# Performance work log

Measured on AMD Instinct MI355X. Metric: run time of the kernel, lower is better.

## Reference

```python
import jax, jax.numpy as jnp
from jax import lax
import numpy as np

# ---- model dims ----
VOCAB, DMODEL, NLAYER = 32000, 1024, 4
NHEAD, HEAD = 16, 64              # RWKV6 heads (DMODEL = NHEAD*HEAD)
DIN = 2 * DMODEL                  # mamba expand=2
MHEAD, MHD = DIN // 64, 64        # mamba heads / head_dim (hard-coded 64 in block)
DSTATE, KCONV = 64, 4             # mamba2 state size / depthwise conv kernel
FFH = 4 * DMODEL
B, T = 1, 1024
EPS = 1e-6


def rmsnorm(v, w):
    return w * v * lax.rsqrt(jnp.mean(v * v, axis=-1, keepdims=True) + EPS)


def causal_dwconv(x, w):
    # x: [B,T,C], w: [C,K] depthwise causal conv
    C, K = w.shape
    xp = jnp.pad(x, ((0, 0), (K - 1, 0), (0, 0)))
    return lax.conv_general_dilated(
        xp, w.T[:, None, :], (1,), 'VALID',
        dimension_numbers=('NWC', 'WIO', 'NWC'), feature_group_count=C)


def setup_inputs() -> dict:
    key = jax.random.key(0)
    ks = iter(jax.random.split(key, 64))
    nrm = lambda shape, s=0.02: jax.random.normal(next(ks), shape, jnp.float32) * s
    x = jax.random.randint(next(ks), (B, T), 0, VOCAB)
    inp = dict(
        x=x,
        embed=nrm((VOCAB, DMODEL)),
        ln_w=jnp.ones((NLAYER, DMODEL), jnp.float32),
        Wr=nrm((NLAYER, DMODEL, DMODEL)), Wk=nrm((NLAYER, DMODEL, DMODEL)),
        Wv=nrm((NLAYER, DMODEL, DMODEL)), Ww=nrm((NLAYER, DMODEL, DMODEL)),
        w_bias=nrm((NLAYER, DMODEL), 0.5), u=nrm((NLAYER, NHEAD, HEAD), 0.5),
        Wg=nrm((NLAYER, DMODEL, DMODEL)), Wo=nrm((NLAYER, DMODEL, DMODEL)),
        Win=nrm((NLAYER, DMODEL, 2 * DIN + 2 * DSTATE + MHEAD)),
        conv_w=nrm((NLAYER, DIN + 2 * DSTATE, KCONV), 0.2),
        dt_bias=nrm((NLAYER, MHEAD), 0.5), A_log=nrm((NLAYER, MHEAD), 0.5),
        Dskip=nrm((NLAYER, MHEAD), 0.5),
        mnorm_w=jnp.ones((NLAYER, DIN), jnp.float32),
        Wout_m=nrm((NLAYER, DIN, DMODEL)),
        gate_w=nrm((NLAYER, 2 * DMODEL)), gate_b=jnp.zeros((NLAYER,), jnp.float32),
        ffn_ln_w=jnp.ones((NLAYER, DMODEL), jnp.float32),
        W1=nrm((NLAYER, DMODEL, FFH)), W2=nrm((NLAYER, FFH, DMODEL)),
        ln_out_w=jnp.ones((DMODEL,), jnp.float32),
    )
    return inp


def _block(h, p):
    (p_ln, pWr, pWk, pWv, pWw, p_wb, p_u, pWg, pWo, pWin, p_cw, p_dtb,
     p_Al, p_D, p_mn, pWom, p_gw, p_gb, p_fln, pW1, pW2) = p
    nx = rmsnorm(h, p_ln)

    # ---- RWKV6 linear attention ----
    r = (nx @ pWr).reshape(B, T, NHEAD, HEAD)
    k = (nx @ pWk).reshape(B, T, NHEAD, HEAD)
    v = (nx @ pWv).reshape(B, T, NHEAD, HEAD)
    dec = jnp.exp(-jnp.exp(nx @ pWw + p_wb)).reshape(B, T, NHEAD, HEAD)  # data-dep decay in (0,1)
    g = jax.nn.silu(nx @ pWg)

    def rstep(S, inp):
        rt, kt, vt, dt_ = inp                      # [B,H,hd]
        kv = kt[..., None] * vt[..., None, :]      # [B,H,hd,hd]
        o = jnp.einsum('bhk,bhkv->bhv', rt, S + p_u[None, :, :, None] * kv)
        return dt_[..., None] * S + kv, o

    S0 = jnp.zeros((B, NHEAD, HEAD, HEAD), nx.dtype)
    tmaj = lambda a: jnp.moveaxis(a, 1, 0)
    _, o = lax.scan(rstep, S0, (tmaj(r), tmaj(k), tmaj(v), tmaj(dec)))
    o = jnp.moveaxis(o, 0, 1).reshape(B, T, DMODEL)
    out_rwkv = (o * g) @ pWo

    # ---- Mamba2 selective scan ----
    zxbcdt = nx @ pWin
    z = zxbcdt[..., :DIN]
    xBC = zxbcdt[..., DIN:2 * DIN + 2 * DSTATE]
    dt = zxbcdt[..., -MHEAD:]
    xBC = jax.nn.silu(causal_dwconv(xBC, p_cw))
    xm = xBC[..., :DIN].reshape(B, T, MHEAD, MHD)
    Bm = xBC[..., DIN:DIN + DSTATE]
    Cm = xBC[..., DIN + DSTATE:]
    dt = jax.nn.softplus(dt + p_dtb)               # [B,T,MH]
    dA = jnp.exp(-dt * jnp.exp(p_Al))              # [B,T,MH]

    def mstep(hst, inp):
        xt, Bt, Ct, dAt, dtt = inp                 # [B,MH,hd],[B,ds],[B,ds],[B,MH],[B,MH]
        hst = dAt[..., None, None] * hst + (dtt[..., None] * xt)[..., None] * Bt[:, None, None, :]
        y = jnp.einsum('bhps,bs->bhp', hst, Ct)
        return hst, y

    h0 = jnp.zeros((B, MHEAD, MHD, DSTATE), nx.dtype)
    _, ym = lax.scan(mstep, h0, (tmaj(xm), tmaj(Bm), tmaj(Cm), tmaj(dA), tmaj(dt)))
    ym = jnp.moveaxis(ym, 0, 1) + p_D[None, None, :, None] * xm
    ym = ym.reshape(B, T, DIN)
    ym = rmsnorm(ym * jax.nn.silu(z), p_mn)        # gated RMSNorm
    out_mamba = ym @ pWom

    # ---- gated fusion + residual + FFN ----
    cat = jnp.concatenate([out_rwkv, out_mamba], axis=-1)
    gate = jax.nn.sigmoid(jnp.einsum('btd,d->bt', cat, p_gw) + p_gb)[..., None]
    h = h + gate * out_rwkv + (1.0 - gate) * out_mamba
    h = h + jax.nn.gelu(rmsnorm(h, p_fln) @ pW1, approximate=False) @ pW2
    return h


def reference(x, embed, ln_w, Wr, Wk, Wv, Ww, w_bias, u, Wg, Wo, Win, conv_w,
              dt_bias, A_log, Dskip, mnorm_w, Wout_m, gate_w, gate_b,
              ffn_ln_w, W1, W2, ln_out_w):
    h = embed[x]  # [B,T,D]
    params = (ln_w, Wr, Wk, Wv, Ww, w_bias, u, Wg, Wo, Win, conv_w, dt_bias,
              A_log, Dskip, mnorm_w, Wout_m, gate_w, gate_b, ffn_ln_w, W1, W2)
    h, _ = lax.scan(lambda c, p: (_block(c, p), None), h, params)
    logits = rmsnorm(h, ln_out_w) @ embed.T  # tied head
    return logits
```

## Files before the change

### kernel.cpp

```cpp
#include <hip/hip_runtime.h>
#include <hip/hip_bf16.h>
#include <math.h>

#define T 1024
#define NLAYER 4
#define NHEAD 16
#define HEAD 64
#define DIN 2048
#define MHEAD 32
#define DSTATE 64
#define FFH 4096
#define NWIN 4256
#define CCONV 2176
#define VOCABSZ 32000
#define NCHUNK 16
#define PKROWS 9472
#define PKN 9376

typedef unsigned short u16;
typedef __attribute__((ext_vector_type(8))) short s16x8;
typedef __attribute__((ext_vector_type(4))) float f32x4;

__device__ inline u16 f2bf(float f) {
  union { float f; unsigned u; } v; v.f = f;
// ... 73 lines not shown
  __shared__ float S[64][65];
  int w = blockIdx.z >> 2, l = blockIdx.z & 3;
  const float* sp = tc.src[w] + (size_t)l * 1024 * 1024;
  u16* dp = tc.dst[w] + (size_t)l * tc.dstride[w];
  int n0 = blockIdx.x * 64, k0 = blockIdx.y * 64;
  int tid = threadIdx.x;
  int tr = tid >> 4, tcc = (tid & 15) * 4;
  #pragma unroll
  for (int it = 0; it < 4; ++it) {
    int r = tr + it * 16;
    float4 v = *(const float4*)&sp[(size_t)(k0 + r) * 1024 + n0 + tcc];
    S[r][tcc + 0] = v.x; S[r][tcc + 1] = v.y; S[r][tcc + 2] = v.z; S[r][tcc + 3] = v.w;
  }
  __syncthreads();
  #pragma unroll
  for (int it = 0; it < 4; ++it) {
    int rn = tr + it * 16;
    u16 o[4];
    o[0] = f2bf(S[tcc + 0][rn]); o[1] = f2bf(S[tcc + 1][rn]);
    o[2] = f2bf(S[tcc + 2][rn]); o[3] = f2bf(S[tcc + 3][rn]);
    *(uint2*)&dp[(size_t)(n0 + rn) * 1024 + k0 + tcc] = *(uint2*)o;
  }
}

__global__ __launch_bounds__(256) void k_embln(const int* x, const float* embed,
                                               const float* w, float* h, u16* out) {
  __shared__ float sb[8];
  int t = blockIdx.x, tid = threadIdx.x;
  int row = x[t];
  float4 v = *(const float4*)&embed[(size_t)row * 1024 + tid * 4];
  *(float4*)&h[(size_t)t * 1024 + tid * 4] = v;
  float ss = v.x * v.x + v.y * v.y + v.z * v.z + v.w * v.w;
  float tot = block_sum(ss, sb);
  float rn = rsqrtf(tot / 1024.f + 1e-6f);
  int c = tid * 4;
  u16 o[4] = {f2bf(v.x * rn * w[c + 0]), f2bf(v.y * rn * w[c + 1]),
              f2bf(v.z * rn * w[c + 2]), f2bf(v.w * rn * w[c + 3])};
  *(uint2*)&out[(size_t)t * 1024 + c] = *(uint2*)o;
}

enum { EPI_F32 = 0, EPI_QKV = 1, EPI_GELU = 2 };

struct GOut {
  void* out;
  const float* aux;
  size_t zstride;
  float *r, *k, *v, *ld, *g, *zx;
};

template <int EPI, int BM, int BN>
__global__ __launch_bounds__(256) void k_gemm2(const u16* __restrict__ A,
                                               const u16* __restrict__ Bt,
                                               int N, int K, int kLen, GOut go) {
  __shared__ __align__(16) u16 As[2][BM][64];
  __shared__ __align__(16) u16 Bs[2][BN][64];
  constexpr int FR = BM / 32, FC = BN / 32;
  constexpr int LPS = BM / 32 + BN / 32;
  int tid = threadIdx.x, lane = tid & 63, wid = tid >> 6;
  int lid = blockIdx.y * gridDim.x + blockIdx.x;
  int nwg = gridDim.x * gridDim.y;
  int q = nwg >> 3, r8 = nwg & 7;
  int xcd = lid & 7, pos = lid >> 3;
  int wg = (xcd < r8) ? (xcd * (q + 1) + pos) : (r8 * (q + 1) + (xcd - r8) * q + pos);
  int m0 = (wg % gridDim.x) * BM, n0 = (wg / gridDim.x) * BN;
  int kOff = blockIdx.z * kLen;
  int wr = (wid >> 1) * (BM / 2), wc = (wid & 1) * (BN / 2);
  int lr = lane & 15, lk8 = (lane >> 4) * 8;
  int rsw = lr & 7;
  int swc = SWZ_SRC(lane);
  int rA = lane >> 3;
  f32x4 acc[FR][FC] = {};

  auto STAGE = [&](int buf, int k0) {
    #pragma unroll
    for (int it = 0; it < BM / 32; ++it) {
      int rb = wid * (BM / 4) + it * 8;
      gload16(&A[(size_t)(m0 + rb + rA) * K + k0 + swc], &As[buf][rb][0]);
    }
    #pragma unroll
    for (int it = 0; it < BN / 32; ++it) {
      int rb = wid * (BN / 4) + it * 8;
      gload16(&Bt[(size_t)(n0 + rb + rA) * K + k0 + swc], &Bs[buf][rb][0]);
    }
  };
  auto COMPUTE = [&](int buf) {
    #pragma unroll
    for (int kb = 0; kb < 64; kb += 32) {
      s16x8 af[FR], bf[FC];
      #pragma unroll
      for (int i = 0; i < FR; ++i)
        af[i] = *(const s16x8*)&As[buf][wr + i * 16 + lr][SWZ_RD(kb, lk8, rsw)];
      #pragma unroll
      for (int j = 0; j < FC; ++j)
        bf[j] = *(const s16x8*)&Bs[buf][wc + j * 16 + lr][SWZ_RD(kb, lk8, rsw)];
      #pragma unroll
      for (int i = 0; i < FR; ++i)
        #pragma unroll
        for (int j = 0; j < FC; ++j)
          acc[i][j] = __builtin_amdgcn_mfma_f32_16x16x32_bf16(af[i], bf[j], acc[i][j], 0, 0, 0);
    }
  };

  int nt = kLen >> 6;
  STAGE(0, kOff);
  int cur = 0;
  for (int t = 0; t < nt; ++t) {
    if (t + 1 < nt) {
      STAGE(cur ^ 1, kOff + (t + 1) * 64);
      asm volatile("s_waitcnt vmcnt(%0)" :: "n"(LPS) : "memory");
    } else {
      asm volatile("s_waitcnt vmcnt(0)" ::: "memory");
    }
    __builtin_amdgcn_s_barrier();
    __builtin_amdgcn_sched_barrier(0);
    COMPUTE(cur);
    __builtin_amdgcn_s_barrier();
    cur ^= 1;
  }

  float* outf = (float*)go.out + (size_t)blockIdx.z * go.zstride;
  #pragma unroll
  for (int i = 0; i < FR; ++i)
    #pragma unroll
    for (int j = 0; j < FC; ++j) {
      int row = m0 + wr + i * 16 + ((lane >> 4) << 2);
      int col = n0 + wc + j * 16 + lr;
      if (col >= N) continue;
      #pragma unroll
      for (int r_ = 0; r_ < 4; ++r_) {
        float v = acc[i][j][r_];
        size_t rr = (size_t)(row + r_);
        if constexpr (EPI == EPI_F32) {
          outf[rr * (size_t)N + col] = v;
        } else if constexpr (EPI == EPI_GELU) {
          ((u16*)go.out)[rr * (size_t)N + col] =
              f2bf(0.5f * v * (1.f + erff(v * 0.70710678118654752f)));
        } else if constexpr (EPI == EPI_QKV) {
          if (col < 1024)       go.r[rr * 1024 + col] = v;
          else if (col < 2048)  go.k[rr * 1024 + col - 1024] = v;
          else if (col < 3072)  go.v[rr * 1024 + col - 2048] = v;
          else if (col < 4096)  go.ld[rr * 1024 + col - 3072] = -expf(v + go.aux[col - 3072]);
          else if (col < 5120)  go.g[rr * 1024 + col - 4096] = v * sigf(v);
          else                  go.zx[rr * 4256 + col - 5120] = v;
        }
      }
    }
}

struct DualArg {
  const u16 *A0, *A1, *B0, *B1;
  float *o0, *o1;
  int K0, K1;
};
__global__ __launch_bounds__(256) void k_dual(DualArg da) {
  __shared__ __align__(16) u16 As[2][64][64];
  __shared__ __align__(16) u16 Bs[2][64][64];
  const u16* A  = blockIdx.z ? da.A1 : da.A0;
  const u16* Bt = blockIdx.z ? da.B1 : da.B0;
  float* out    = blockIdx.z ? da.o1 : da.o0;
  int K         = blockIdx.z ? da.K1 : da.K0;
  const int N = 1024;
  int tid = threadIdx.x, lane = tid & 63, wid = tid >> 6;
  int lid = blockIdx.y * gridDim.x + blockIdx.x;
  int nwg = gridDim.x * gridDim.y;
  int q = nwg >> 3, r8 = nwg & 7;
  int xcd = lid & 7, pos = lid >> 3;
  int wg = (xcd < r8) ? (xcd * (q + 1) + pos) : (r8 * (q + 1) + (xcd - r8) * q + pos);
  int m0 = (wg % gridDim.x) * 64, n0 = (wg / gridDim.x) * 64;
  int wr = (wid >> 1) * 32, wc = (wid & 1) * 32;
  int lr = lane & 15, lk8 = (lane >> 4) * 8;
  int rsw = lr & 7, swc = SWZ_SRC(lane), rA = lane >> 3;
  f32x4 acc[2][2] = {};
  auto STAGE = [&](int buf, int k0) {
    #pragma unroll
    for (int it = 0; it < 2; ++it) {
      int rb = wid * 16 + it * 8;
      gload16(&A[(size_t)(m0 + rb + rA) * K + k0 + swc], &As[buf][rb][0]);
      gload16(&Bt[(size_t)(n0 + rb + rA) * K + k0 + swc], &Bs[buf][rb][0]);
    }
  };
  auto COMPUTE = [&](int buf) {
    #pragma unroll
    for (int kb = 0; kb < 64; kb += 32) {
      s16x8 af[2], bf[2];
      #pragma unroll
      for (int i = 0; i < 2; ++i)
        af[i] = *(const s16x8*)&As[buf][wr + i * 16 + lr][SWZ_RD(kb, lk8, rsw)];
      #pragma unroll
      for (int j = 0; j < 2; ++j)
        bf[j] = *(const s16x8*)&Bs[buf][wc + j * 16 + lr][SWZ_RD(kb, lk8, rsw)];
      #pragma unroll
      for (int i = 0; i < 2; ++i)
        #pragma unroll
        for (int j = 0; j < 2; ++j)
          acc[i][j] = __builtin_amdgcn_mfma_f32_16x16x32_bf16(af[i], bf[j], acc[i][j], 0, 0, 0);
    }
  };
  int nt = K >> 6;
  STAGE(0, 0);
  int cur = 0;
  for (int t = 0; t < nt; ++t) {
    if (t + 1 < nt) {
      STAGE(cur ^ 1, (t + 1) * 64);
      asm volatile("s_waitcnt vmcnt(4)" ::: "memory");
    } else {
      asm volatile("s_waitcnt vmcnt(0)" ::: "memory");
    }
    __builtin_amdgcn_s_barrier();
    __builtin_amdgcn_sched_barrier(0);
    COMPUTE(cur);
    __builtin_amdgcn_s_barrier();
    cur ^= 1;
  }
  #pragma unroll
  for (int i = 0; i < 2; ++i)
    #pragma unroll
    for (int j = 0; j < 2; ++j) {
      int row = m0 + wr + i * 16 + ((lane >> 4) << 2);
      int col = n0 + wc + j * 16 + lr;
      #pragma unroll
      for (int r_ = 0; r_ < 4; ++r_)
        out[(size_t)(row + r_) * N + col] = acc[i][j][r_];
    }
}

__global__ void k_conv(const float* zx, const float* cw, float* xc) {
  int c = blockIdx.x * 256 + threadIdx.x;
  int t = blockIdx.y;
  if (c >= CCONV) return;
  float4 w = *(const float4*)&cw[c * 4];
  float acc = 0.f;
  if (t - 3 >= 0) acc += zx[(size_t)(t - 3) * NWIN + 2048 + c] * w.x;
  if (t - 2 >= 0) acc += zx[(size_t)(t - 2) * NWIN + 2048 + c] * w.y;
  if (t - 1 >= 0) acc += zx[(size_t)(t - 1) * NWIN + 2048 + c] * w.z;
  acc += zx[(size_t)t * NWIN + 2048 + c] * w.w;
  xc[(size_t)t * CCONV + c] = acc * sigf(acc);
}

__global__ __launch_bounds__(256) void k_dtbc(const float* __restrict__ zx,
                                              const float* __restrict__ xc,
                                              const float* __restrict__ dt_bias,
                                              const float* __restrict__ A_log,
                                              float* __restrict__ dtb, float* __restrict__ la,
                                              float* __restrict__ BC) {
  __shared__ float ldaS[64][33];
  __shared__ float Bc[64][65], Cc[64][65];
  int c = blockIdx.x, tid = threadIdx.x;
  #pragma unroll
  for (int it = 0; it < 8; ++it) {
    int e = it * 256 + tid;
    int i = e >> 5, j = e & 31;
    float x = zx[(size_t)(c * 64 + i) * NWIN + 4224 + j] + dt_bias[j];
    float sp = (x > 20.f) ? x : log1pf(expf(x));
    dtb[(size_t)(c * 64 + i) * 32 + j] = sp;
    ldaS[i][j] = -sp * expf(A_log[j]);
  }
  #pragma unroll
  for (int it = 0; it < 4; ++it) {
    int idx = it * 256 + tid;
    int r = idx >> 4, c4 = (idx & 15) * 4;
    float4 b4 = *(const float4*)&xc[(size_t)(c * 64 + r) * CCONV + 2048 + c4];
    float4 cv = *(const float4*)&xc[(size_t)(c * 64 + r) * CCONV + 2112 + c4];
    Bc[r][c4] = b4.x; Bc[r][c4+1] = b4.y; Bc[r][c4+2] = b4.z; Bc[r][c4+3] = b4.w;
    Cc[r][c4] = cv.x; Cc[r][c4+1] = cv.y; Cc[r][c4+2] = cv.z; Cc[r][c4+3] = cv.w;
  }
  __syncthreads();
  if (tid < 32) {
    float g = 0.f;
    for (int i = 0; i < 64; ++i) {
      g += ldaS[i][tid];
      la[((size_t)c * 32 + tid) * 64 + i] = g;
    }
  }
  int i = tid & 63, sg = tid >> 6;
  float acc[16] = {};
  for (int d = 0; d < 64; ++d) {
    float cv = Cc[i][d];
    #pragma unroll
    for (int j = 0; j < 16; ++j) acc[j] += Bc[sg * 16 + j][d] * cv;
  }
  #pragma unroll
  for (int j = 0; j < 16; ++j)
    BC[((size_t)c * 64 + i) * 64 + sg * 16 + j] = acc[j];
}

union SmemH1 {
  struct { float rS[64][66], kS[64][66], gS[64][66]; u16 khS[64][64]; u16 vtS[64][72]; float uS[64]; } a;
  struct { u16 XT[64][72], BT[64][72]; float fS[64]; } b;
};
__global__ __launch_bounds__(256) void k_heads1(const float* __restrict__ rbuf,
                                                const float* __restrict__ kbuf,
                                                const float* __restrict__ ldbuf,
                                                const float* __restrict__ vbuf,
                                                const float* __restrict__ u,
                                                const float* __restrict__ xc,
                                                const float* __restrict__ la,
                                                const float* __restrict__ dtb,
                                                u16* __restrict__ rt, float* __restrict__ eL,
                                                u16* __restrict__ G, float* __restrict__ U,
                                                float* __restrict__ Um) {
  __shared__ SmemH1 sm;
  int c = blockIdx.x, tid = threadIdx.x;
  int lane = tid & 63, wid = tid >> 6;
  int lr = lane & 15, lk8 = (lane >> 4) * 8, rsw = lr & 7;
  int wr = (wid >> 1) * 32, wc = (wid & 1) * 32;
  if (blockIdx.y < 16) {
    int h = blockIdx.y;
    #pragma unroll
    for (int it = 0; it < 4; ++it) {
      int idx = it * 256 + tid;
      int i = idx >> 4, c4 = (idx & 15) * 4;
      size_t base = (size_t)(c * 64 + i) * 1024 + h * 64 + c4;
      float4 rv = *(const float4*)&rbuf[base];
      float4 kv = *(const float4*)&kbuf[base];
      float4 lv = *(const float4*)&ldbuf[base];
      float4 vv = *(const float4*)&vbuf[base];
      sm.a.rS[i][c4] = rv.x; sm.a.rS[i][c4+1] = rv.y; sm.a.rS[i][c4+2] = rv.z; sm.a.rS[i][c4+3] = rv.w;
      sm.a.kS[i][c4] = kv.x; sm.a.kS[i][c4+1] = kv.y; sm.a.kS[i][c4+2] = kv.z; sm.a.kS[i][c4+3] = kv.w;
      sm.a.gS[i][c4] = lv.x; sm.a.gS[i][c4+1] = lv.y; sm.a.gS[i][c4+2] = lv.z; sm.a.gS[i][c4+3] = lv.w;
      sm.a.vtS[c4 + 0][i] = f2bf(vv.x); sm.a.vtS[c4 + 1][i] = f2bf(vv.y);
      sm.a.vtS[c4 + 2][i] = f2bf(vv.z); sm.a.vtS[c4 + 3][i] = f2bf(vv.w);
    }
    if (tid < 64) sm.a.uS[tid] = u[h * 64 + tid];
    __syncthreads();
    if (tid < 64) {
      int k = tid;
      float g = 0.f;
      for (int i = 0; i < 64; ++i) {
        float ld = sm.a.gS[i][k];
        sm.a.gS[i][k] = g;
        rt[(size_t)(c * 64 + i) * 1024 + h * 64 + k] = f2bf(sm.a.rS[i][k] * expf(g));
        g += ld;
      }
      float gL = g;
      eL[((size_t)c * 16 + h) * 64 + k] = expf(gL);
      for (int i = 0; i < 64; ++i) {
        float gincl = (i < 63) ? sm.a.gS[i + 1][k] : gL;
        int col = (((i >> 3) ^ (k & 7)) << 3) | (i & 7);
        sm.a.khS[k][col] = f2bf(sm.a.kS[i][k] * expf(fminf(gL - gincl, 0.f)));
      }
    }
    __syncthreads();
    {
      int i = tid & 63, sg = tid >> 6;
      float acc[16] = {};
      float accd = 0.f;
      for (int k = 0; k < 64; ++k) {
        float rv = sm.a.rS[i][k], gi = sm.a.gS[i][k];
        accd += rv * sm.a.uS[k] * sm.a.kS[i][k];
        #pragma unroll
        for (int j = 0; j < 16; ++j) {
          int s = sg * 16 + j;
          int sp1 = (s < 63) ? s + 1 : 63;
          acc[j] += rv * sm.a.kS[s][k] * expf(fminf(gi - sm.a.gS[sp1][k], 0.f));
        }
      }
      #pragma unroll
      for (int j = 0; j < 16; ++j) {
        int s = sg * 16 + j;
        float v = (s < i) ? acc[j] : ((s == i) ? accd : 0.f);
        G[(((size_t)c * 16 + h) * 64 + i) * 64 + s] = f2bf(v);
      }
    }
    {
      size_t gb = ((size_t)c * 16 + h) * 64;
      f32x4 acc2[2][2] = {};
      #pragma unroll
      for (int kb = 0; kb < 64; kb += 32) {
        s16x8 a[2], b[2];
        #pragma unroll
        for (int i_ = 0; i_ < 2; ++i_)
          a[i_] = *(const s16x8*)&sm.a.khS[wr + i_ * 16 + lr][SWZ_RD(kb, lk8, rsw)];
        #pragma unroll
        for (int j_ = 0; j_ < 2; ++j_)
          b[j_] = *(const s16x8*)&sm.a.vtS[wc + j_ * 16 + lr][kb + lk8];
        #pragma unroll
        for (int i_ = 0; i_ < 2; ++i_)
          #pragma unroll
          for (int j_ = 0; j_ < 2; ++j_)
            acc2[i_][j_] = __builtin_amdgcn_mfma_f32_16x16x32_bf16(a[i_], b[j_], acc2[i_][j_], 0, 0, 0);
      }
      #pragma unroll
      for (int i_ = 0; i_ < 2; ++i_)
        #pragma unroll
        for (int j_ = 0; j_ < 2; ++j_) {
          int row = wr + i_ * 16 + ((lane >> 4) << 2);
          int col = wc + j_ * 16 + lr;
          #pragma unroll
          for (int r_ = 0; r_ < 4; ++r_)
            U[(gb + row + r_) * 64 + col] = acc2[i_][j_][r_];
        }
    }
  } else {
    int h = blockIdx.y - 16;
    size_t lb = ((size_t)c * 32 + h) * 64;
    if (tid < 64) {
      float la63 = la[lb + 63];
      sm.b.fS[tid] = dtb[(size_t)(c * 64 + tid) * 32 + h] * expf(fminf(la63 - la[lb + tid], 0.f));
    }
    __syncthreads();
    #pragma unroll
    for (int it = 0; it < 4; ++it) {
      int idx = it * 256 + tid;
      int t = idx >> 4, p4 = (idx & 15) * 4;
      float f = sm.b.fS[t];
      float4 xv = *(const float4*)&xc[(size_t)(c * 64 + t) * CCONV + h * 64 + p4];
      sm.b.XT[p4 + 0][t] = f2bf(f * xv.x); sm.b.XT[p4 + 1][t] = f2bf(f * xv.y);
      sm.b.XT[p4 + 2][t] = f2bf(f * xv.z); sm.b.XT[p4 + 3][t] = f2bf(f * xv.w);
      float4 bv = *(const float4*)&xc[(size_t)(c * 64 + t) * CCONV + 2048 + p4];
      sm.b.BT[p4 + 0][t] = f2bf(bv.x); sm.b.BT[p4 + 1][t] = f2bf(bv.y);
      sm.b.BT[p4 + 2][t] = f2bf(bv.z); sm.b.BT[p4 + 3][t] = f2bf(bv.w);
    }
    __syncthreads();
    f32x4 acc[2][2] = {};
    #pragma unroll
    for (int kb = 0; kb < 64; kb += 32) {
      s16x8 a[2], b[2];
      #pragma unroll
      for (int i = 0; i < 2; ++i) a[i] = *(const s16x8*)&sm.b.XT[wr + i * 16 + lr][kb + lk8];
      #pragma unroll
      for (int j = 0; j < 2; ++j) b[j] = *(const s16x8*)&sm.b.BT[wc + j * 16 + lr][kb + lk8];
      #pragma unroll
      for (int i = 0; i < 2; ++i)
        #pragma unroll
        for (int j = 0; j < 2; ++j)
          acc[i][j] = __builtin_amdgcn_mfma_f32_16x16x32_bf16(a[i], b[j], acc[i][j], 0, 0, 0);
    }
    #pragma unroll
    for (int i = 0; i < 2; ++i)
      #pragma unroll
      for (int j = 0; j < 2; ++j) {
        int row = wr + i * 16 + ((lane >> 4) << 2);
        int col = wc + j * 16 + lr;
        #pragma unroll
        for (int r_ = 0; r_ < 4; ++r_)
          Um[(lb + row + r_) * 64 + col] = acc[i][j][r_];
      }
  }
}

__global__ __launch_bounds__(256) void k_scan2(const float* __restrict__ Urw,
                                               const float* __restrict__ eL,
                                               u16* __restrict__ Sall,
                                               const float* __restrict__ Um,
                                               const float* __restrict__ la,
                                               u16* __restrict__ hall) {
  int tid = threadIdx.x;
  if (blockIdx.x < 16) {
    int h = blockIdx.x;
    int k = tid >> 2, v0 = blockIdx.y * 16 + (tid & 3) * 4;
    float S[4] = {};
    for (int c = 0; c < 16; ++c) {
      size_t gb = ((size_t)c * 16 + h) * 64;
      u16 tmp[4] = {f2bf(S[0]), f2bf(S[1]), f2bf(S[2]), f2bf(S[3])};
      *(uint2*)&Sall[(gb + k) * 64 + v0] = *(uint2*)&tmp[0];
      float e = eL[gb + k];
      float4 uv = *(const float4*)&Urw[(gb + k) * 64 + v0];
      S[0] = e * S[0] + uv.x; S[1] = e * S[1] + uv.y;
      S[2] = e * S[2] + uv.z; S[3] = e * S[3] + uv.w;
    }
  } else {
    int h = blockIdx.x - 16;
    int p = tid >> 2, s0 = blockIdx.y * 16 + (tid & 3) * 4;
    float S[4] = {};
    for (int c = 0; c < 16; ++c) {
      size_t lb = ((size_t)c * 32 + h) * 64;
      u16 tmp[4] = {f2bf(S[0]), f2bf(S[1]), f2bf(S[2]), f2bf(S[3])};
      *(uint2*)&hall[(lb + p) * 64 + s0] = *(uint2*)&tmp[0];
      float e = expf(la[lb + 63]);
      float4 uv = *(const float4*)&Um[(lb + p) * 64 + s0];
      S[0] = e * S[0] + uv.x; S[1] = e * S[1] + uv.y;
      S[2] = e * S[2] + uv.z; S[3] = e * S[3] + uv.w;
    }
  }
}

union SmemH2 {
  struct { u16 rtS[64][64], GS[64][64], StS[64][72], vtS[64][72]; } a;
  struct { u16 MS[64][64], hS[64][64], CtS[64][72], XT2[64][72]; float laS[64], dtbS[64], eS[64]; } b;
};
__global__ __launch_bounds__(256) void k_heads2(const u16* __restrict__ rt,
                                                const u16* __restrict__ Gb,
                                                const u16* __restrict__ Sall,
                                                const float* __restrict__ vbuf,
                                                const float* __restrict__ gbuf,
                                                u16* __restrict__ og,
                                                const u16* __restrict__ hall,
                                                const float* __restrict__ xc,
                                                const float* __restrict__ la,
                                                const float* __restrict__ dtb,
                                                const float* __restrict__ BC,
                                                float* __restrict__ ymb) {
  __shared__ SmemH2 sm;
  int c = blockIdx.x, tid = threadIdx.x;
  int lane = tid & 63, wid = tid >> 6;
  int lr = lane & 15, lk8 = (lane >> 4) * 8;
  int rsw = lr & 7, swc = SWZ_SRC(lane);
  int wr = (wid >> 1) * 32, wc = (wid & 1) * 32;
  if (blockIdx.y < 16) {
    int h = blockIdx.y;
    size_t gb = ((size_t)c * 16 + h) * 64;
    #pragma unroll
    for (int it = 0; it < 2; ++it) {
      int rb = wid * 16 + it * 8;
      int r = rb + (lane >> 3);
      gload16(&rt[(size_t)(c * 64 + r) * 1024 + h * 64 + swc], &sm.a.rtS[rb][0]);
      gload16(&Gb[(gb + r) * 64 + swc], &sm.a.GS[rb][0]);
    }
    #pragma unroll
    for (int it = 0; it < 2; ++it) {
      int idx = it * 256 + tid;
      int k = idx >> 3, c8 = (idx & 7) * 8;
      uint4 ld = *(const uint4*)&Sall[(gb + k) * 64 + c8];
      const u16* pv = (const u16*)&ld;
      #pragma unroll
      for (int jj = 0; jj < 8; ++jj) sm.a.StS[c8 + jj][k] = pv[jj];
    }
    #pragma unroll
    for (int it = 0; it < 4; ++it) {
      int idx = it * 256 + tid;
      int s = idx >> 4, v4 = (idx & 15) * 4;
      float4 vv = *(const float4*)&vbuf[(size_t)(c * 64 + s) * 1024 + h * 64 + v4];
      sm.a.vtS[v4 + 0][s] = f2bf(vv.x); sm.a.vtS[v4 + 1][s] = f2bf(vv.y);
      sm.a.vtS[v4 + 2][s] = f2bf(vv.z); sm.a.vtS[v4 + 3][s] = f2bf(vv.w);
    }
    __syncthreads();
    f32x4 acc[2][2] = {};
    #pragma unroll
    for (int kb = 0; kb < 64; kb += 32) {
      s16x8 aR[2], aG[2], bS[2], bV[2];
      #pragma unroll
      for (int i = 0; i < 2; ++i) {
        aR[i] = *(const s16x8*)&sm.a.rtS[wr + i * 16 + lr][SWZ_RD(kb, lk8, rsw)];
        aG[i] = *(const s16x8*)&sm.a.GS[wr + i * 16 + lr][SWZ_RD(kb, lk8, rsw)];
      }
      #pragma unroll
      for (int j = 0; j < 2; ++j) {
        bS[j] = *(const s16x8*)&sm.a.StS[wc + j * 16 + lr][kb + lk8];
        bV[j] = *(const s16x8*)&sm.a.vtS[wc + j * 16 + lr][kb + lk8];
      }
      #pragma unroll
      for (int i = 0; i < 2; ++i)
        #pragma unroll
        for (int j = 0; j < 2; ++j) {
          acc[i][j] = __builtin_amdgcn_mfma_f32_16x16x32_bf16(aR[i], bS[j], acc[i][j], 0, 0, 0);
          acc[i][j] = __builtin_amdgcn_mfma_f32_16x16x32_bf16(aG[i], bV[j], acc[i][j], 0, 0, 0);
        }
    }
    #pragma unroll
    for (int i = 0; i < 2; ++i)
      #pragma unroll
      for (int j = 0; j < 2; ++j) {
        int row = c * 64 + wr + i * 16 + ((lane >> 4) << 2);
        int col = h * 64 + wc + j * 16 + lr;
        #pragma unroll
        for (int r_ = 0; r_ < 4; ++r_) {
          size_t idx = (size_t)(row + r_) * 1024 + col;
          og[idx] = f2bf(acc[i][j][r_] * gbuf[idx]);
        }
      }
  } else {
    int h = blockIdx.y - 16;
    size_t lb = ((size_t)c * 32 + h) * 64;
    if (tid < 64) {
      float lv = la[lb + tid];
      sm.b.laS[tid] = lv;
      sm.b.eS[tid] = expf(lv);
      sm.b.dtbS[tid] = dtb[(size_t)(c * 64 + tid) * 32 + h];
    }
    #pragma unroll
    for (int it = 0; it < 2; ++it) {
      int rb = wid * 16 + it * 8;
      int r = rb + (lane >> 3);
      gload16(&hall[(lb + r) * 64 + swc], &sm.b.hS[rb][0]);
    }
    __syncthreads();
    #pragma unroll
    for (int it = 0; it < 4; ++it) {
      int idx = it * 256 + tid;
      int i = idx >> 4, s4 = (idx & 15) * 4;
      float lai = sm.b.laS[i];
      float4 bc4 = *(const float4*)&BC[((size_t)c * 64 + i) * 64 + s4];
      u16 mo[4];
      #pragma unroll
      for (int j = 0; j < 4; ++j) {
        int s = s4 + j;
        float bcv = (j == 0) ? bc4.x : (j == 1) ? bc4.y : (j == 2) ? bc4.z : bc4.w;
        float v = 0.f;
        if (s <= i)
          v = expf(fminf(lai - sm.b.laS[s], 0.f)) * sm.b.dtbS[s] * bcv;
        mo[j] = f2bf(v);
      }
      *(uint2*)&sm.b.MS[i][(((s4 >> 3) ^ (i & 7)) << 3) | (s4 & 7)] = *(uint2*)mo;
      float ei = sm.b.eS[i];
      float4 cv = *(const float4*)&xc[(size_t)(c * 64 + i) * CCONV + 2112 + s4];
      sm.b.CtS[i][s4 + 0] = f2bf(ei * cv.x); sm.b.CtS[i][s4 + 1] = f2bf(ei * cv.y);
      sm.b.CtS[i][s4 + 2] = f2bf(ei * cv.z); sm.b.CtS[i][s4 + 3] = f2bf(ei * cv.w);
      float4 xv = *(const float4*)&xc[(size_t)(c * 64 + i) * CCONV + h * 64 + s4];
      sm.b.XT2[s4 + 0][i] = f2bf(xv.x); sm.b.XT2[s4 + 1][i] = f2bf(xv.y);
      sm.b.XT2[s4 + 2][i] = f2bf(xv.z); sm.b.XT2[s4 + 3][i] = f2bf(xv.w);
    }
    __syncthreads();
    f32x4 acc[2][2] = {};
    #pragma unroll
    for (int kb = 0; kb < 64; kb += 32) {
      s16x8 aM[2], aC[2], bX[2], bH[2];
      #pragma unroll
      for (int i = 0; i < 2; ++i) {
        aM[i] = *(const s16x8*)&sm.b.MS[wr + i * 16 + lr][SWZ_RD(kb, lk8, rsw)];
        aC[i] = *(const s16x8*)&sm.b.CtS[wr + i * 16 + lr][kb + lk8];
      }
      #pragma unroll
      for (int j = 0; j < 2; ++j) {
        bX[j] = *(const s16x8*)&sm.b.XT2[wc + j * 16 + lr][kb + lk8];
        bH[j] = *(const s16x8*)&sm.b.hS[wc + j * 16 + lr][SWZ_RD(kb, lk8, rsw)];
      }
      #pragma unroll
      for (int i = 0; i < 2; ++i)
        #pragma unroll
        for (int j = 0; j < 2; ++j) {
          acc[i][j] = __builtin_amdgcn_mfma_f32_16x16x32_bf16(aM[i], bX[j], acc[i][j], 0, 0, 0);
          acc[i][j] = __builtin_amdgcn_mfma_f32_16x16x32_bf16(aC[i], bH[j], acc[i][j], 0, 0, 0);
        }
    }
    #pragma unroll
    for (int i = 0; i < 2; ++i)
      #pragma unroll
      for (int j = 0; j < 2; ++j) {
        int row = c * 64 + wr + i * 16 + ((lane >> 4) << 2);
        int col = h * 64 + wc + j * 16 + lr;
        #pragma unroll
        for (int r_ = 0; r_ < 4; ++r_)
          ymb[(size_t)(row + r_) * 2048 + col] = acc[i][j][r_];
      }
  }
}

__global__ __launch_bounds__(256) void k_ymn(const float* ymb, const float* xc,
                                             const float* zx, const float* Dsk,
                                             const float* mnw, u16* out) {
  __shared__ float sb[8];
  int t = blockIdx.x, tid = threadIdx.x;
  float vals[8];
// ... 118 lines not shown
  float* rbuf     = (float*)alloc((size_t)T * 1024 * 4);
  float* kbuf     = (float*)alloc((size_t)T * 1024 * 4);
  float* vbuf     = (float*)alloc((size_t)T * 1024 * 4);
  float* ldbuf    = (float*)alloc((size_t)T * 1024 * 4);
  float* gbuf     = (float*)alloc((size_t)T * 1024 * 4);
  float* zx       = (float*)alloc((size_t)T * NWIN * 4);
  u16*   rt       = (u16*)alloc((size_t)T * 1024 * 2);
  float* eL       = (float*)alloc((size_t)NCHUNK * 16 * 64 * 4);
  u16*   Gb       = (u16*)alloc((size_t)NCHUNK * 16 * 64 * 64 * 2);
  float* Urw      = (float*)alloc((size_t)NCHUNK * 16 * 64 * 64 * 4);
  u16*   Sall     = (u16*)alloc((size_t)NCHUNK * 16 * 64 * 64 * 2);
  u16*   og       = (u16*)alloc((size_t)T * 1024 * 2);
  float* out_rwkv = (float*)alloc((size_t)T * 1024 * 4);
  float* xc       = (float*)alloc((size_t)T * CCONV * 4);
  float* dtb      = (float*)alloc((size_t)T * 32 * 4);
  float* la       = (float*)alloc((size_t)NCHUNK * 32 * 64 * 4);
  float* BC       = (float*)alloc((size_t)NCHUNK * 64 * 64 * 4);
  float* Um       = (float*)alloc((size_t)NCHUNK * 32 * 64 * 64 * 4);
  u16*   hall     = (u16*)alloc((size_t)NCHUNK * 32 * 64 * 64 * 2);
  float* ymb      = (float*)alloc((size_t)T * 2048 * 4);
  u16*   ymn      = (u16*)alloc((size_t)T * 2048 * 2);
  float* out_mam  = (float*)alloc((size_t)T * 1024 * 4);
  u16*   ffa      = (u16*)alloc((size_t)T * FFH * 2);
  float* part     = (float*)alloc((size_t)4 * 1024 * 1024 * 4);

  const size_t PKS = (size_t)PKROWS * 1024;

  k_cast<<<VOCABSZ * 1024 / 1024, 256, 0, stream>>>(embed, embB);
  {
    TC6 tc;
    tc.src[0] = Wr; tc.src[1] = Wk; tc.src[2] = Wv; tc.src[3] = Ww; tc.src[4] = Wg; tc.src[5] = Wo;
    tc.dst[0] = Wpk;               tc.dstride[0] = PKS;
    tc.dst[1] = Wpk + 1024 * 1024; tc.dstride[1] = PKS;
    tc.dst[2] = Wpk + 2048 * 1024; tc.dstride[2] = PKS;
    tc.dst[3] = Wpk + 3072 * 1024; tc.dstride[3] = PKS;
    tc.dst[4] = Wpk + 4096 * 1024; tc.dstride[4] = PKS;
    tc.dst[5] = WoT;               tc.dstride[5] = (size_t)1024 * 1024;
    k_tcast6<<<dim3(16, 16, 24), 256, 0, stream>>>(tc);
  }
  k_tcast<<<dim3(67, 16, 4), 256, 0, stream>>>(Win, (size_t)1024 * NWIN, Wpk + (size_t)5120 * 1024, PKS, 1024, NWIN);
  k_tcast<<<dim3(16, 32, 4), 256, 0, stream>>>(Wout_m, (size_t)2048 * 1024, WomT, (size_t)1024 * 2048, 2048, 1024);
  k_tcast<<<dim3(64, 16, 4), 256, 0, stream>>>(W1, (size_t)1024 * 4096, W1T, (size_t)4096 * 1024, 1024, 4096);
  k_tcast<<<dim3(16, 64, 4), 256, 0, stream>>>(W2, (size_t)4096 * 1024, W2T, (size_t)1024 * 4096, 4096, 1024);

  k_embln<<<1024, 256, 0, stream>>>(x, embed, ln_w, h, nx);

  for (int l = 0; l < NLAYER; ++l) {
    {
      GOut go = {};
      go.r = rbuf; go.k = kbuf; go.v = vbuf; go.ld = ldbuf; go.g = gbuf; go.zx = zx;
      go.aux = w_bias + l * 1024;
      k_gemm2<EPI_QKV, 128, 128><<<dim3(8, 74), 256, 0, stream>>>(nx, Wpk + (size_t)l * PKS, PKN, 1024, 1024, go);
    }
    k_conv<<<dim3(9, 1024), 256, 0, stream>>>(zx, conv_w + (size_t)l * CCONV * 4, xc);
    k_dtbc<<<16, 256, 0, stream>>>(zx, xc, dt_bias + l * 32, A_log + l * 32, dtb, la, BC);
    k_heads1<<<dim3(16, 48), 256, 0, stream>>>(rbuf, kbuf, ldbuf, vbuf, u + (size_t)l * 1024,
                                               xc, la, dtb, rt, eL, Gb, Urw, Um);
    k_scan2<<<dim3(48, 4), 256, 0, stream>>>(Urw, eL, Sall, Um, la, hall);
    k_heads2<<<dim3(16, 48), 256, 0, stream>>>(rt, Gb, Sall, vbuf, gbuf, og,
                                               hall, xc, la, dtb, BC, ymb);
    k_ymn<<<1024, 256, 0, stream>>>(ymb, xc, zx, Dskip + l * 32, mnorm_w + (size_t)l * 2048, ymn);
    {
      DualArg da;
      da.A0 = og;  da.B0 = WoT + (size_t)l * 1024 * 1024;  da.o0 = out_rwkv; da.K0 = 1024;
      da.A1 = ymn; da.B1 = WomT + (size_t)l * 1024 * 2048; da.o1 = out_mam;  da.K1 = 2048;
      k_dual<<<dim3(16, 16, 2), 256, 0, stream>>>(da);
    }
    k_gateln<<<1024, 256, 0, stream>>>(out_rwkv, out_mam, gate_w + (size_t)l * 2048,
                                       gate_b + l, h, ffn_ln + l * 1024, nx);
    {
      GOut go = {}; go.out = ffa;
      k_gemm2<EPI_GELU, 128, 128><<<dim3(8, 32), 256, 0, stream>>>(nx, W1T + (size_t)l * 4096 * 1024, 4096, 1024, 1024, go);
    }
    {
      GOut go = {}; go.out = part; go.zstride = (size_t)1024 * 1024;
      k_gemm2<EPI_F32, 64, 64><<<dim3(16, 16, 4), 256, 0, stream>>>(ffa, W2T + (size_t)l * 1024 * 4096, 1024, 4096, 1024, go);
    }
    k_redln<<<1024, 256, 0, stream>>>(part, h,
                                      (l < NLAYER - 1) ? (ln_w + (l + 1) * 1024) : ln_out, nx);
  }

  {
    GOut go = {}; go.out = d_out;
    k_gemm2<EPI_F32, 128, 128><<<dim3(8, 250), 256, 0, stream>>>(nx, embB, VOCABSZ, 1024, 1024, go);
  }
}
```

Before: 1.215 ms.

## Stage GEMM epilogues through shared memory, vectorize conv, split dtbc, use fast exp

GEMM kernels now merge their A and B shared buffers into one array. That array is reused after the main loop to stage the accumulator tile, so the epilogue can write coalesced float4 or bf16x4 rows instead of scattered scalar stores. The depthwise conv handles four channels per thread with float4 loads and stores. The dtbc kernel is split into five blocks per chunk so the B·C product is spread across more workgroups. Several expf calls in the scan kernels become __expf, which may cost some accuracy.

```diff
diff --git a/kernel.cpp b/kernel.cpp
--- a/kernel.cpp
+++ b/kernel.cpp
@@ -149,8 +149,7 @@
 __global__ __launch_bounds__(256) void k_gemm2(const u16* __restrict__ A,
                                                const u16* __restrict__ Bt,
                                                int N, int K, int kLen, GOut go) {
-  __shared__ __align__(16) u16 As[2][BM][64];
-  __shared__ __align__(16) u16 Bs[2][BN][64];
+  __shared__ __align__(16) u16 smem[2][BM + BN][64];
   constexpr int FR = BM / 32, FC = BN / 32;
   constexpr int LPS = BM / 32 + BN / 32;
   int tid = threadIdx.x, lane = tid & 63, wid = tid >> 6;
@@ -172,12 +171,12 @@
     #pragma unroll
     for (int it = 0; it < BM / 32; ++it) {
       int rb = wid * (BM / 4) + it * 8;
-      gload16(&A[(size_t)(m0 + rb + rA) * K + k0 + swc], &As[buf][rb][0]);
+      gload16(&A[(size_t)(m0 + rb + rA) * K + k0 + swc], &smem[buf][rb][0]);
     }
     #pragma unroll
     for (int it = 0; it < BN / 32; ++it) {
       int rb = wid * (BN / 4) + it * 8;
-      gload16(&Bt[(size_t)(n0 + rb + rA) * K + k0 + swc], &Bs[buf][rb][0]);
+      gload16(&Bt[(size_t)(n0 + rb + rA) * K + k0 + swc], &smem[buf][BM + rb][0]);
     }
   };
   auto COMPUTE = [&](int buf) {
@@ -186,10 +185,10 @@
       s16x8 af[FR], bf[FC];
       #pragma unroll
       for (int i = 0; i < FR; ++i)
-        af[i] = *(const s16x8*)&As[buf][wr + i * 16 + lr][SWZ_RD(kb, lk8, rsw)];
+        af[i] = *(const s16x8*)&smem[buf][wr + i * 16 + lr][SWZ_RD(kb, lk8, rsw)];
       #pragma unroll
       for (int j = 0; j < FC; ++j)
-        bf[j] = *(const s16x8*)&Bs[buf][wc + j * 16 + lr][SWZ_RD(kb, lk8, rsw)];
+        bf[j] = *(const s16x8*)&smem[buf][BM + wc + j * 16 + lr][SWZ_RD(kb, lk8, rsw)];
       #pragma unroll
       for (int i = 0; i < FR; ++i)
         #pragma unroll
@@ -215,33 +214,86 @@
     cur ^= 1;
   }
 
-  float* outf = (float*)go.out + (size_t)blockIdx.z * go.zstride;
+  __syncthreads();
+  float* cbuf = (float*)&smem[0][0][0];
   #pragma unroll
   for (int i = 0; i < FR; ++i)
     #pragma unroll
     for (int j = 0; j < FC; ++j) {
-      int row = m0 + wr + i * 16 + ((lane >> 4) << 2);
-      int col = n0 + wc + j * 16 + lr;
-      if (col >= N) continue;
-      #pragma unroll
-      for (int r_ = 0; r_ < 4; ++r_) {
-        float v = acc[i][j][r_];
-        size_t rr = (size_t)(row + r_);
-        if constexpr (EPI == EPI_F32) {
-          outf[rr * (size_t)N + col] = v;
-        } else if constexpr (EPI == EPI_GELU) {
-          ((u16*)go.out)[rr * (size_t)N + col] =
-              f2bf(0.5f * v * (1.f + erff(v * 0.70710678118654752f)));
-        } else if constexpr (EPI == EPI_QKV) {
-          if (col < 1024)       go.r[rr * 1024 + col] = v;
-          else if (col < 2048)  go.k[rr * 1024 + col - 1024] = v;
-          else if (col < 3072)  go.v[rr * 1024 + col - 2048] = v;
-          else if (col < 4096)  go.ld[rr * 1024 + col - 3072] = -expf(v + go.aux[col - 3072]);
-          else if (col < 5120)  go.g[rr * 1024 + col - 4096] = v * sigf(v);
-          else                  go.zx[rr * 4256 + col - 5120] = v;
-        }
-      }
-    }
+      int rrow = wr + i * 16 + ((lane >> 4) << 2);
+      int ccol = wc + j * 16 + lr;
+      #pragma unroll
+      for (int r_ = 0; r_ < 4; ++r_)
+        cbuf[(rrow + r_) * BN + ccol] = acc[i][j][r_];
+    }
+  __syncthreads();
+  constexpr int RPB = BN / 4;
+  constexpr int ITERS = (BM * RPB) / 256;
+  if constexpr (EPI == EPI_F32) {
+    float* outf = (float*)go.out + (size_t)blockIdx.z * go.zstride;
+    #pragma unroll
+    for (int it2 = 0; it2 < ITERS; ++it2) {
+      int idx = it2 * 256 + tid;
+      int row = idx / RPB, c4 = (idx % RPB) * 4;
+      int gc = n0 + c4;
+      if (gc >= N) continue;
+      float4 v = *(const float4*)&cbuf[row * BN + c4];
+      if (gc + 3 < N) *(float4*)&outf[(size_t)(m0 + row) * N + gc] = v;
+      else {
+        const float* pv = (const float*)&v;
+        for (int e = 0; e < 4 && gc + e < N; ++e)
+          outf[(size_t)(m0 + row) * N + gc + e] = pv[e];
+      }
+    }
+  } else if constexpr (EPI == EPI_GELU) {
+    u16* outb = (u16*)go.out;
+    #pragma unroll
+    for (int it2 = 0; it2 < ITERS; ++it2) {
+      int idx = it2 * 256 + tid;
+      int row = idx / RPB, c4 = (idx % RPB) * 4;
+      int gc = n0 + c4;
+      if (gc + 3 >= N) continue;
+      float4 v = *(const float4*)&cbuf[row * BN + c4];
+      u16 o[4];
+      o[0] = f2bf(0.5f * v.x * (1.f + erff(v.x * 0.70710678118654752f)));
+      o[1] = f2bf(0.5f * v.y * (1.f + erff(v.y * 0.70710678118654752f)));
+      o[2] = f2bf(0.5f * v.z * (1.f + erff(v.z * 0.70710678118654752f)));
+      o[3] = f2bf(0.5f * v.w * (1.f + erff(v.w * 0.70710678118654752f)));
+      *(uint2*)&outb[(size_t)(m0 + row) * N + gc] = *(uint2*)o;
+    }
+  } else {
+    float* tptr; int ldbw, coff, op;
+    if (n0 < 5120) {
+      int tsel = n0 >> 10;
+      tptr = (tsel == 0) ? go.r : (tsel == 1) ? go.k : (tsel == 2) ? go.v
+           : (tsel == 3) ? go.ld : go.g;
+      ldbw = 1024; coff = n0 & 1023;
+      op = (tsel == 3) ? 1 : (tsel == 4) ? 2 : 0;
+    } else {
+      tptr = go.zx; ldbw = 4256; coff = n0 - 5120; op = 0;
+    }
+    #pragma unroll
+    for (int it2 = 0; it2 < ITERS; ++it2) {
+      int idx = it2 * 256 + tid;
+      int row = idx / RPB, c4 = (idx % RPB) * 4;
+      int gc = n0 + c4;
+      if (gc >= N) continue;
+      float4 v = *(const float4*)&cbuf[row * BN + c4];
+      float* pv = (float*)&v;
+      if (op == 1) {
+        #pragma unroll
+        for (int e = 0; e < 4; ++e) pv[e] = -expf(pv[e] + go.aux[coff + c4 + e]);
+      } else if (op == 2) {
+        #pragma unroll
+        for (int e = 0; e < 4; ++e) pv[e] = pv[e] * sigf(pv[e]);
+      }
+      if (gc + 3 < N) *(float4*)&tptr[(size_t)(m0 + row) * ldbw + coff + c4] = v;
+      else {
+        for (int e = 0; e < 4 && gc + e < N; ++e)
+          tptr[(size_t)(m0 + row) * ldbw + coff + c4 + e] = pv[e];
+      }
+    }
+  }
 }
 
 struct DualArg {
@@ -250,8 +302,7 @@
   int K0, K1;
 };
 __global__ __launch_bounds__(256) void k_dual(DualArg da) {
-  __shared__ __align__(16) u16 As[2][64][64];
-  __shared__ __align__(16) u16 Bs[2][64][64];
+  __shared__ __align__(16) u16 smem[2][128][64];
   const u16* A  = blockIdx.z ? da.A1 : da.A0;
   const u16* Bt = blockIdx.z ? da.B1 : da.B0;
   float* out    = blockIdx.z ? da.o1 : da.o0;
@@ -272,8 +323,8 @@
     #pragma unroll
     for (int it = 0; it < 2; ++it) {
       int rb = wid * 16 + it * 8;
-      gload16(&A[(size_t)(m0 + rb + rA) * K + k0 + swc], &As[buf][rb][0]);
-      gload16(&Bt[(size_t)(n0 + rb + rA) * K + k0 + swc], &Bs[buf][rb][0]);
+      gload16(&A[(size_t)(m0 + rb + rA) * K + k0 + swc], &smem[buf][rb][0]);
+      gload16(&Bt[(size_t)(n0 + rb + rA) * K + k0 + swc], &smem[buf][64 + rb][0]);
     }
   };
   auto COMPUTE = [&](int buf) {
@@ -282,10 +333,10 @@
       s16x8 af[2], bf[2];
       #pragma unroll
       for (int i = 0; i < 2; ++i)
-        af[i] = *(const s16x8*)&As[buf][wr + i * 16 + lr][SWZ_RD(kb, lk8, rsw)];
+        af[i] = *(const s16x8*)&smem[buf][wr + i * 16 + lr][SWZ_RD(kb, lk8, rsw)];
       #pragma unroll
       for (int j = 0; j < 2; ++j)
-        bf[j] = *(const s16x8*)&Bs[buf][wc + j * 16 + lr][SWZ_RD(kb, lk8, rsw)];
+        bf[j] = *(const s16x8*)&smem[buf][64 + wc + j * 16 + lr][SWZ_RD(kb, lk8, rsw)];
       #pragma unroll
       for (int i = 0; i < 2; ++i)
         #pragma unroll
@@ -309,29 +360,51 @@
     __builtin_amdgcn_s_barrier();
     cur ^= 1;
   }
+  __syncthreads();
+  float* cbuf = (float*)&smem[0][0][0];
   #pragma unroll
   for (int i = 0; i < 2; ++i)
     #pragma unroll
     for (int j = 0; j < 2; ++j) {
-      int row = m0 + wr + i * 16 + ((lane >> 4) << 2);
-      int col = n0 + wc + j * 16 + lr;
+      int rrow = wr + i * 16 + ((lane >> 4) << 2);
+      int ccol = wc + j * 16 + lr;
       #pragma unroll
       for (int r_ = 0; r_ < 4; ++r_)
-        out[(size_t)(row + r_) * N + col] = acc[i][j][r_];
-    }
-}
-
-__global__ void k_conv(const float* zx, const float* cw, float* xc) {
-  int c = blockIdx.x * 256 + threadIdx.x;
+        cbuf[(rrow + r_) * 64 + ccol] = acc[i][j][r_];
+    }
+  __syncthreads();
+  #pragma unroll
+  for (int it2 = 0; it2 < 4; ++it2) {
+    int idx = it2 * 256 + tid;
+    int row = idx >> 4, c4 = (idx & 15) * 4;
+    *(float4*)&out[(size_t)(m0 + row) * N + n0 + c4] = *(const float4*)&cbuf[row * 64 + c4];
+  }
+}
+
+__global__ __launch_bounds__(256) void k_conv(const float* __restrict__ zx,
+                                              const float* __restrict__ cw,
+                                              float* __restrict__ xc) {
+  int c = (blockIdx.x * 256 + threadIdx.x) * 4;
   int t = blockIdx.y;
   if (c >= CCONV) return;
-  float4 w = *(const float4*)&cw[c * 4];
-  float acc = 0.f;
-  if (t - 3 >= 0) acc += zx[(size_t)(t - 3) * NWIN + 2048 + c] * w.x;
-  if (t - 2 >= 0) acc += zx[(size_t)(t - 2) * NWIN + 2048 + c] * w.y;
-  if (t - 1 >= 0) acc += zx[(size_t)(t - 1) * NWIN + 2048 + c] * w.z;
-  acc += zx[(size_t)t * NWIN + 2048 + c] * w.w;
-  xc[(size_t)t * CCONV + c] = acc * sigf(acc);
+  float4 w0 = *(const float4*)&cw[(c + 0) * 4];
+  float4 w1 = *(const float4*)&cw[(c + 1) * 4];
+  float4 w2 = *(const float4*)&cw[(c + 2) * 4];
+  float4 w3 = *(const float4*)&cw[(c + 3) * 4];
+  float4 a = {0.f, 0.f, 0.f, 0.f};
+  #pragma unroll
+  for (int tap = 0; tap < 4; ++tap) {
+    int tt = t - 3 + tap;
+    if (tt < 0) continue;
+    float4 z = *(const float4*)&zx[(size_t)tt * NWIN + 2048 + c];
+    a.x += z.x * ((const float*)&w0)[tap];
+    a.y += z.y * ((const float*)&w1)[tap];
+    a.z += z.z * ((const float*)&w2)[tap];
+    a.w += z.w * ((const float*)&w3)[tap];
+  }
+  a.x = a.x * sigf(a.x); a.y = a.y * sigf(a.y);
+  a.z = a.z * sigf(a.z); a.w = a.w * sigf(a.w);
+  *(float4*)&xc[(size_t)t * CCONV + c] = a;
 }
 
 __global__ __launch_bounds__(256) void k_dtbc(const float* __restrict__ zx,
@@ -340,45 +413,54 @@
                                               const float* __restrict__ A_log,
                                               float* __restrict__ dtb, float* __restrict__ la,
                                               float* __restrict__ BC) {
-  __shared__ float ldaS[64][33];
-  __shared__ float Bc[64][65], Cc[64][65];
   int c = blockIdx.x, tid = threadIdx.x;
-  #pragma unroll
-  for (int it = 0; it < 8; ++it) {
-    int e = it * 256 + tid;
-    int i = e >> 5, j = e & 31;
-    float x = zx[(size_t)(c * 64 + i) * NWIN + 4224 + j] + dt_bias[j];
-    float sp = (x > 20.f) ? x : log1pf(expf(x));
-    dtb[(size_t)(c * 64 + i) * 32 + j] = sp;
-    ldaS[i][j] = -sp * expf(A_log[j]);
-  }
-  #pragma unroll
-  for (int it = 0; it < 4; ++it) {
-    int idx = it * 256 + tid;
-    int r = idx >> 4, c4 = (idx & 15) * 4;
-    float4 b4 = *(const float4*)&xc[(size_t)(c * 64 + r) * CCONV + 2048 + c4];
-    float4 cv = *(const float4*)&xc[(size_t)(c * 64 + r) * CCONV + 2112 + c4];
-    Bc[r][c4] = b4.x; Bc[r][c4+1] = b4.y; Bc[r][c4+2] = b4.z; Bc[r][c4+3] = b4.w;
-    Cc[r][c4] = cv.x; Cc[r][c4+1] = cv.y; Cc[r][c4+2] = cv.z; Cc[r][c4+3] = cv.w;
-  }
-  __syncthreads();
-  if (tid < 32) {
-    float g = 0.f;
-    for (int i = 0; i < 64; ++i) {
-      g += ldaS[i][tid];
-      la[((size_t)c * 32 + tid) * 64 + i] = g;
-    }
-  }
-  int i = tid & 63, sg = tid >> 6;
-  float acc[16] = {};
-  for (int d = 0; d < 64; ++d) {
-    float cv = Cc[i][d];
-    #pragma unroll
-    for (int j = 0; j < 16; ++j) acc[j] += Bc[sg * 16 + j][d] * cv;
-  }
-  #pragma unroll
-  for (int j = 0; j < 16; ++j)
-    BC[((size_t)c * 64 + i) * 64 + sg * 16 + j] = acc[j];
+  if (blockIdx.y == 0) {
+    __shared__ float ldaS[64][33];
+    #pragma unroll
+    for (int it = 0; it < 8; ++it) {
+      int e = it * 256 + tid;
+      int i = e >> 5, j = e & 31;
+      float x = zx[(size_t)(c * 64 + i) * NWIN + 4224 + j] + dt_bias[j];
+      float sp = (x > 20.f) ? x : log1pf(expf(x));
+      dtb[(size_t)(c * 64 + i) * 32 + j] = sp;
+      ldaS[i][j] = -sp * expf(A_log[j]);
+    }
+    __syncthreads();
+    if (tid < 32) {
+      float g = 0.f;
+      for (int i = 0; i < 64; ++i) {
+        g += ldaS[i][tid];
+        la[((size_t)c * 32 + tid) * 64 + i] = g;
+      }
+    }
+  } else {
+    __shared__ float Bc[64][65];
+    __shared__ float Cc[16][65];
+    int i0 = (blockIdx.y - 1) * 16;
+    #pragma unroll
+    for (int it = 0; it < 4; ++it) {
+      int idx = it * 256 + tid;
+      int r = idx >> 4, c4 = (idx & 15) * 4;
+      float4 b4 = *(const float4*)&xc[(size_t)(c * 64 + r) * CCONV + 2048 + c4];
+      Bc[r][c4] = b4.x; Bc[r][c4+1] = b4.y; Bc[r][c4+2] = b4.z; Bc[r][c4+3] = b4.w;
+    }
+    {
+      int r = tid >> 4, c4 = (tid & 15) * 4;
+      float4 cv = *(const float4*)&xc[(size_t)(c * 64 + i0 + r) * CCONV + 2112 + c4];
+      Cc[r][c4] = cv.x; Cc[r][c4+1] = cv.y; Cc[r][c4+2] = cv.z; Cc[r][c4+3] = cv.w;
+    }
+    __syncthreads();
+    int il = tid >> 4, sg = tid & 15;
+    float acc[4] = {};
+    for (int d = 0; d < 64; ++d) {
+      float cv = Cc[il][d];
+      #pragma unroll
+      for (int j = 0; j < 4; ++j) acc[j] += Bc[sg * 4 + j][d] * cv;
+    }
+    #pragma unroll
+    for (int j = 0; j < 4; ++j)
+      BC[((size_t)c * 64 + i0 + il) * 64 + sg * 4 + j] = acc[j];
+  }
 }
 
 union SmemH1 {
@@ -426,15 +508,15 @@
       for (int i = 0; i < 64; ++i) {
         float ld = sm.a.gS[i][k];
         sm.a.gS[i][k] = g;
-        rt[(size_t)(c * 64 + i) * 1024 + h * 64 + k] = f2bf(sm.a.rS[i][k] * expf(g));
+        rt[(size_t)(c * 64 + i) * 1024 + h * 64 + k] = f2bf(sm.a.rS[i][k] * __expf(g));
         g += ld;
       }
       float gL = g;
-      eL[((size_t)c * 16 + h) * 64 + k] = expf(gL);
+      eL[((size_t)c * 16 + h) * 64 + k] = __expf(gL);
       for (int i = 0; i < 64; ++i) {
         float gincl = (i < 63) ? sm.a.gS[i + 1][k] : gL;
         int col = (((i >> 3) ^ (k & 7)) << 3) | (i & 7);
-        sm.a.khS[k][col] = f2bf(sm.a.kS[i][k] * expf(fminf(gL - gincl, 0.f)));
+        sm.a.khS[k][col] = f2bf(sm.a.kS[i][k] * __expf(fminf(gL - gincl, 0.f)));
       }
     }
     __syncthreads();
@@ -449,7 +531,7 @@
         for (int j = 0; j < 16; ++j) {
           int s = sg * 16 + j;
           int sp1 = (s < 63) ? s + 1 : 63;
-          acc[j] += rv * sm.a.kS[s][k] * expf(fminf(gi - sm.a.gS[sp1][k], 0.f));
+          acc[j] += rv * sm.a.kS[s][k] * __expf(fminf(gi - sm.a.gS[sp1][k], 0.f));
         }
       }
       #pragma unroll
@@ -493,7 +575,7 @@
     size_t lb = ((size_t)c * 32 + h) * 64;
     if (tid < 64) {
       float la63 = la[lb + 63];
-      sm.b.fS[tid] = dtb[(size_t)(c * 64 + tid) * 32 + h] * expf(fminf(la63 - la[lb + tid], 0.f));
+      sm.b.fS[tid] = dtb[(size_t)(c * 64 + tid) * 32 + h] * __expf(fminf(la63 - la[lb + tid], 0.f));
     }
     __syncthreads();
     #pragma unroll
@@ -564,7 +646,7 @@
       size_t lb = ((size_t)c * 32 + h) * 64;
       u16 tmp[4] = {f2bf(S[0]), f2bf(S[1]), f2bf(S[2]), f2bf(S[3])};
       *(uint2*)&hall[(lb + p) * 64 + s0] = *(uint2*)&tmp[0];
-      float e = expf(la[lb + 63]);
+      float e = __expf(la[lb + 63]);
       float4 uv = *(const float4*)&Um[(lb + p) * 64 + s0];
       S[0] = e * S[0] + uv.x; S[1] = e * S[1] + uv.y;
       S[2] = e * S[2] + uv.z; S[3] = e * S[3] + uv.w;
@@ -662,7 +744,7 @@
     if (tid < 64) {
       float lv = la[lb + tid];
       sm.b.laS[tid] = lv;
-      sm.b.eS[tid] = expf(lv);
+      sm.b.eS[tid] = __expf(lv);
       sm.b.dtbS[tid] = dtb[(size_t)(c * 64 + tid) * 32 + h];
     }
     #pragma unroll
@@ -685,7 +767,7 @@
         float bcv = (j == 0) ? bc4.x : (j == 1) ? bc4.y : (j == 2) ? bc4.z : bc4.w;
         float v = 0.f;
         if (s <= i)
-          v = expf(fminf(lai - sm.b.laS[s], 0.f)) * sm.b.dtbS[s] * bcv;
+          v = __expf(fminf(lai - sm.b.laS[s], 0.f)) * sm.b.dtbS[s] * bcv;
         mo[j] = f2bf(v);
       }
       *(uint2*)&sm.b.MS[i][(((s4 >> 3) ^ (i & 7)) << 3) | (s4 & 7)] = *(uint2*)mo;
@@ -910,8 +992,8 @@
       go.aux = w_bias + l * 1024;
       k_gemm2<EPI_QKV, 128, 128><<<dim3(8, 74), 256, 0, stream>>>(nx, Wpk + (size_t)l * PKS, PKN, 1024, 1024, go);
     }
-    k_conv<<<dim3(9, 1024), 256, 0, stream>>>(zx, conv_w + (size_t)l * CCONV * 4, xc);
-    k_dtbc<<<16, 256, 0, stream>>>(zx, xc, dt_bias + l * 32, A_log + l * 32, dtb, la, BC);
+    k_conv<<<dim3(3, 1024), 256, 0, stream>>>(zx, conv_w + (size_t)l * CCONV * 4, xc);
+    k_dtbc<<<dim3(16, 5), 256, 0, stream>>>(zx, xc, dt_bias + l * 32, A_log + l * 32, dtb, la, BC);
     k_heads1<<<dim3(16, 48), 256, 0, stream>>>(rbuf, kbuf, ldbuf, vbuf, u + (size_t)l * 1024,
                                                xc, la, dtb, rt, eL, Gb, Urw, Um);
     k_scan2<<<dim3(48, 4), 256, 0, stream>>>(Urw, eL, Sall, Um, la, hall);
```

Measured after the change: 1.106 ms. 1.1x faster.
